# Kernel tuning notes

Hardware: AMD Instinct MI355X
Metric: run time of the kernel (lower is better)

The kernel has to match this reference:

```python
import jax, jax.numpy as jnp
import numpy as np


def setup_inputs() -> dict:
    key = jax.random.key(0)
    k1, k2 = jax.random.split(key)
    B, C, H, W, F = 32, 256, 64, 64, 256
    inputs = jax.random.normal(k1, (B, C, H, W), dtype=jnp.float32)
    biases = jax.random.normal(k2, (1, 1, C, F), dtype=jnp.float32)
    return {"inputs": inputs, "biases": biases}


def _mix_weights(biases):
    # UnitSphereInit.get_log_prob: unit-sphere parameterization of a
    # probability vector over input channels: p_cf = b_cf^2 / sum_c b_cf^2.
    # The original computes log(p) and later exponentiates inside logsumexp;
    # we keep p directly (same math, fewer transcendentals).
    sq = biases * biases                      # (1,1,C,F)
    p = sq / jnp.sum(sq, axis=2, keepdims=True)
    return p.reshape(biases.shape[2], biases.shape[3])  # (C, F)


def reference(inputs, biases):
    # out[b,f,h,w] = logsumexp_c( x[b,c,h,w] + log p[c,f] )
    #             = m[b,h,w] + log( sum_c exp(x - m) * p[c,f] )
    # p <= 1 so the exp is safe; the channel reduction over all filters
    # fuses into one GEMM (single pass over the input, all filters at once).
    p = _mix_weights(biases)                          # (C, F)
    m = jnp.max(inputs, axis=1, keepdims=True)        # (B,1,H,W)
    e = jnp.exp(inputs - m)                           # (B,C,H,W)
    s = jnp.einsum('bchw,cf->bfhw', e, p)             # (B,F,H,W)
    return m + jnp.log(s)
```

## Files before the change

kernel.cpp:

```cpp
#include <hip/hip_runtime.h>
#include <stdint.h>

#define C_DIM  256
#define F_DIM  256
#define HW     4096
#define JT     64
#define NCHUNK 8

typedef __attribute__((ext_vector_type(8))) short   bf16x8;
typedef __attribute__((ext_vector_type(4))) float   floatx4;

__device__ __forceinline__ unsigned short f32_to_bf16(float f) {
    union { float f; unsigned int u; } v; v.f = f;
    unsigned int u = v.u;
    return (unsigned short)((u + 0x7FFFu + ((u >> 16) & 1u)) >> 16);
}

__global__ void prep_kernel(const float* __restrict__ b,
                            unsigned short* __restrict__ apack) {
    __shared__ float part[16][17];
    __shared__ float inv_s[16];
    const int t     = threadIdx.x;
    const int ftile = blockIdx.x;
    const int f0    = ftile * 16;

    const int fl = t & 15;
    const int cg = t >> 4;
    float s = 0.f;
#pragma unroll
    for (int k = 0; k < 16; ++k) {
        float v = b[(cg + 16 * k) * F_DIM + f0 + fl];
        s += v * v;
    }
    part[cg][fl] = s;
    __syncthreads();
    if (t < 16) {
        float acc = 0.f;
#pragma unroll
        for (int g = 0; g < 16; ++g) acc += part[g][t];
        inv_s[t] = 1.0f / acc;
    }
    __syncthreads();

#pragma unroll
    for (int e = t; e < 512; e += 256) {
        const int kiter = e >> 6;
        const int lane  = e & 63;
        const int f     = f0 + (lane & 15);
        const int c0    = kiter * 32 + ((lane >> 4) << 3);
        const float inv = inv_s[lane & 15];
        bf16x8 v;
#pragma unroll
        for (int i = 0; i < 8; ++i) {
            float w = b[(c0 + i) * F_DIM + f];
            v[i] = (short)f32_to_bf16(w * w * inv);
        }
        *(bf16x8*)(apack + ((size_t)(ftile * 8 + kiter) * 64 + lane) * 8) = v;
    }
}

__global__ __launch_bounds__(256, 4)
void mixture_kernel(const float* __restrict__ x,
                    const unsigned short* __restrict__ apack,
                    float* __restrict__ out) {
    const int t     = threadIdx.x;
    const int wv    = t >> 6;
    const int lane  = t & 63;
    const int llo   = lane & 15;
    const int lhi   = lane >> 4;
    const int fg    = wv & 1;
    const int jg    = wv >> 1;
    const int batch = blockIdx.x >> 6;
    const int hw0   = (blockIdx.x & 63) * JT;

    const float* xl = x + (size_t)batch * C_DIM * HW
                        + (size_t)(lhi * 8) * HW + hw0 + jg * 32 + llo;

    const bf16x8* ap = (const bf16x8*)apack;

    floatx4 acc[8][2];
#pragma unroll
    for (int ft = 0; ft < 8; ++ft)
#pragma unroll
        for (int jj = 0; jj < 2; ++jj)
            acc[ft][jj] = (floatx4){0.f, 0.f, 0.f, 0.f};

    float xc[2][8];
#pragma unroll
    for (int jj = 0; jj < 2; ++jj)
#pragma unroll
        for (int q = 0; q < 8; ++q)
            xc[jj][q] = xl[(size_t)q * HW + jj * 16];

#pragma unroll
    for (int ck = 0; ck < NCHUNK; ++ck) {
        float xn[2][8];
        if (ck < NCHUNK - 1) {
#pragma unroll
            for (int jj = 0; jj < 2; ++jj)
#pragma unroll
                for (int q = 0; q < 8; ++q)
                    xn[jj][q] = xl[(size_t)((ck + 1) * 32 + q) * HW + jj * 16];
        }

        bf16x8 bfr[2];
#pragma unroll
        for (int jj = 0; jj < 2; ++jj)
#pragma unroll
            for (int q = 0; q < 8; ++q)
                bfr[jj][q] = (short)f32_to_bf16(__expf(xc[jj][q]));

#pragma unroll
        for (int ft = 0; ft < 8; ++ft) {
            bf16x8 af = ap[((size_t)(fg * 8 + ft) * 8 + ck) * 64 + lane];
            acc[ft][0] = __builtin_amdgcn_mfma_f32_16x16x32_bf16(
                af, bfr[0], acc[ft][0], 0, 0, 0);
            acc[ft][1] = __builtin_amdgcn_mfma_f32_16x16x32_bf16(
                af, bfr[1], acc[ft][1], 0, 0, 0);
        }

        if (ck < NCHUNK - 1) {
#pragma unroll
            for (int jj = 0; jj < 2; ++jj)
#pragma unroll
                for (int q = 0; q < 8; ++q)
                    xc[jj][q] = xn[jj][q];
        }
    }

    float* ob = out + (size_t)batch * F_DIM * HW + hw0 + jg * 32 + llo;
#pragma unroll
    for (int ft = 0; ft < 8; ++ft) {
        const int fbase = (fg * 8 + ft) * 16 + lhi * 4;
#pragma unroll
        for (int r = 0; r < 4; ++r) {
            float* orow = ob + (size_t)(fbase + r) * HW;
#pragma unroll
            for (int jj = 0; jj < 2; ++jj)
                orow[jj * 16] = __logf(acc[ft][jj][r]);
        }
    }
}

extern "C" void kernel_launch(void* const* d_in, const int* in_sizes, int n_in,
                              void* d_out, int out_size, void* d_ws, size_t ws_size,
                              hipStream_t stream) {
    const float* x      = (const float*)d_in[0];
    const float* biases = (const float*)d_in[1];
    float* out = (float*)d_out;

    unsigned short* apack = (unsigned short*)d_ws;

    prep_kernel<<<16, 256, 0, stream>>>(biases, apack);
    mixture_kernel<<<2048, 256, 0, stream>>>(x, apack, out);
}
```

Before: 291.5 us.

## Stage exp(x) tile in LDS and swap MFMA operands for vectorized stores

The mixture kernel now uses 512-thread blocks over a 128-pixel tile. It computes exp(x) once per element into a padded bf16 LDS tile, then each wave loops over its filter tiles, reading B fragments from LDS. MFMA operands are swapped so each lane holds four consecutive pixels, which allows float4 output stores instead of scalar ones. The aim is to share the exp work and input reads across all filters in a block, at the cost of about 66KB of LDS per block, a full barrier, and no overlap between loading and the matrix math.

```diff
diff --git a/kernel.cpp b/kernel.cpp
--- a/kernel.cpp
+++ b/kernel.cpp
@@ -4,8 +4,8 @@
 #define C_DIM  256
 #define F_DIM  256
 #define HW     4096
-#define JT     64
-#define NCHUNK 8
+#define TW     128
+#define ETP    264
 
 typedef __attribute__((ext_vector_type(8))) short   bf16x8;
 typedef __attribute__((ext_vector_type(4))) float   floatx4;
@@ -59,85 +59,76 @@
     }
 }
 
-__global__ __launch_bounds__(256, 4)
+__global__ __launch_bounds__(512, 4)
 void mixture_kernel(const float* __restrict__ x,
                     const unsigned short* __restrict__ apack,
                     float* __restrict__ out) {
+    __shared__ __align__(16) unsigned short et[TW][ETP];
+
     const int t     = threadIdx.x;
     const int wv    = t >> 6;
     const int lane  = t & 63;
     const int llo   = lane & 15;
     const int lhi   = lane >> 4;
-    const int fg    = wv & 1;
-    const int jg    = wv >> 1;
-    const int batch = blockIdx.x >> 6;
-    const int hw0   = (blockIdx.x & 63) * JT;
+    const int batch = blockIdx.x >> 5;
+    const int hw0   = (blockIdx.x & 31) * TW;
 
-    const float* xl = x + (size_t)batch * C_DIM * HW
-                        + (size_t)(lhi * 8) * HW + hw0 + jg * 32 + llo;
+    const int j  = t & 127;
+    const int cg = t >> 7;
+
+    const float* xb = x + (size_t)batch * C_DIM * HW + hw0 + j;
+
+#pragma unroll
+    for (int r = 0; r < 8; ++r) {
+        const int c0 = r * 32 + cg * 8;
+        float xv[8];
+#pragma unroll
+        for (int q = 0; q < 8; ++q)
+            xv[q] = xb[(size_t)(c0 + q) * HW];
+        bf16x8 v;
+#pragma unroll
+        for (int q = 0; q < 8; ++q)
+            v[q] = (short)f32_to_bf16(__expf(xv[q]));
+        *(bf16x8*)&et[j][c0] = v;
+    }
+
+    __syncthreads();
 
     const bf16x8* ap = (const bf16x8*)apack;
-
-    floatx4 acc[8][2];
-#pragma unroll
-    for (int ft = 0; ft < 8; ++ft)
-#pragma unroll
-        for (int jj = 0; jj < 2; ++jj)
-            acc[ft][jj] = (floatx4){0.f, 0.f, 0.f, 0.f};
-
-    float xc[2][8];
-#pragma unroll
-    for (int jj = 0; jj < 2; ++jj)
-#pragma unroll
-        for (int q = 0; q < 8; ++q)
-            xc[jj][q] = xl[(size_t)q * HW + jj * 16];
+    float* obase = out + (size_t)batch * F_DIM * HW + hw0 + lhi * 4;
 
 #pragma unroll
-    for (int ck = 0; ck < NCHUNK; ++ck) {
-        float xn[2][8];
-        if (ck < NCHUNK - 1) {
+    for (int rr = 0; rr < 2; ++rr) {
+        const int ft = wv * 2 + rr;
+
+        bf16x8 af[8];
 #pragma unroll
-            for (int jj = 0; jj < 2; ++jj)
+        for (int ks = 0; ks < 8; ++ks)
+            af[ks] = ap[((size_t)ft * 8 + ks) * 64 + lane];
+
+        floatx4 acc[8];
 #pragma unroll
-                for (int q = 0; q < 8; ++q)
-                    xn[jj][q] = xl[(size_t)((ck + 1) * 32 + q) * HW + jj * 16];
+        for (int jt = 0; jt < 8; ++jt)
+            acc[jt] = (floatx4){0.f, 0.f, 0.f, 0.f};
+
+#pragma unroll
+        for (int ks = 0; ks < 8; ++ks) {
+#pragma unroll
+            for (int jt = 0; jt < 8; ++jt) {
+                bf16x8 bfrag =
+                    *(const bf16x8*)&et[jt * 16 + llo][ks * 32 + lhi * 8];
+                acc[jt] = __builtin_amdgcn_mfma_f32_16x16x32_bf16(
+                    bfrag, af[ks], acc[jt], 0, 0, 0);
+            }
         }
 
-        bf16x8 bfr[2];
+        float* orow = obase + (size_t)(ft * 16 + llo) * HW;
 #pragma unroll
-        for (int jj = 0; jj < 2; ++jj)
+        for (int jt = 0; jt < 8; ++jt) {
+            floatx4 o;
 #pragma unroll
-            for (int q = 0; q < 8; ++q)
-                bfr[jj][q] = (short)f32_to_bf16(__expf(xc[jj][q]));
-
-#pragma unroll
-        for (int ft = 0; ft < 8; ++ft) {
-            bf16x8 af = ap[((size_t)(fg * 8 + ft) * 8 + ck) * 64 + lane];
-            acc[ft][0] = __builtin_amdgcn_mfma_f32_16x16x32_bf16(
-                af, bfr[0], acc[ft][0], 0, 0, 0);
-            acc[ft][1] = __builtin_amdgcn_mfma_f32_16x16x32_bf16(
-                af, bfr[1], acc[ft][1], 0, 0, 0);
-        }
-
-        if (ck < NCHUNK - 1) {
-#pragma unroll
-            for (int jj = 0; jj < 2; ++jj)
-#pragma unroll
-                for (int q = 0; q < 8; ++q)
-                    xc[jj][q] = xn[jj][q];
-        }
-    }
-
-    float* ob = out + (size_t)batch * F_DIM * HW + hw0 + jg * 32 + llo;
-#pragma unroll
-    for (int ft = 0; ft < 8; ++ft) {
-        const int fbase = (fg * 8 + ft) * 16 + lhi * 4;
-#pragma unroll
-        for (int r = 0; r < 4; ++r) {
-            float* orow = ob + (size_t)(fbase + r) * HW;
-#pragma unroll
-            for (int jj = 0; jj < 2; ++jj)
-                orow[jj * 16] = __logf(acc[ft][jj][r]);
+            for (int k4 = 0; k4 < 4; ++k4) o[k4] = __logf(acc[jt][k4]);
+            *(floatx4*)(orow + jt * 16) = o;
         }
     }
 }
@@ -152,5 +143,5 @@
     unsigned short* apack = (unsigned short*)d_ws;
 
     prep_kernel<<<16, 256, 0, stream>>>(biases, apack);
-    mixture_kernel<<<2048, 256, 0, stream>>>(x, apack, out);
+    mixture_kernel<<<1024, 512, 0, stream>>>(x, apack, out);
 }
```

Measured after the change: 255.9 us. -12.2%, faster.
